# Kernel optimization log

Measured on AMD Instinct MI355X. Metric: run time of the kernel, lower is better.

## Reference

```python
import jax, jax.numpy as jnp
import numpy as np

POOL = 7      # AdaptiveMaxPool2d output size
CROP = 96     # max box side; all generated boxes fit inside a CROP x CROP window


def _adaptive_maxpool_box(feature_chw, coord):
    """PyTorch AdaptiveMaxPool2d((7,7)) on feature_chw[:, y1:y2, x1:x2].

    feature_chw: [2, H, W]; coord: int32 [4] = (y1, x1, y2, x2), with
    0 < y2-y1 <= CROP, 0 < x2-x1 <= CROP. Returns [2, 7, 7].
    """
    y1, x1, y2, x2 = coord[0], coord[1], coord[2], coord[3]
    crop = jax.lax.dynamic_slice(feature_chw, (0, y1, x1), (2, CROP, CROP))
    h = y2 - y1
    w = x2 - x1
    i = jnp.arange(POOL)
    r = jnp.arange(CROP)
    # PyTorch adaptive pooling bins: [floor(i*h/P), ceil((i+1)*h/P))
    sr = (i * h) // POOL
    er = ((i + 1) * h + POOL - 1) // POOL
    sc = (i * w) // POOL
    ec = ((i + 1) * w + POOL - 1) // POOL
    mask_r = (r[None, :] >= sr[:, None]) & (r[None, :] < er[:, None])  # [7, CROP]
    mask_c = (r[None, :] >= sc[:, None]) & (r[None, :] < ec[:, None])  # [7, CROP]
    neg = jnp.finfo(crop.dtype).min
    # row-wise max per output row: [7, 2, CROP]
    rowp = jnp.max(jnp.where(mask_r[:, None, :, None], crop[None], neg), axis=2)
    # col-wise max per output col: [7, 7, 2]
    out = jnp.max(jnp.where(mask_c[None, :, None, :], rowp[:, None], neg), axis=3)
    return jnp.transpose(out, (2, 0, 1))  # [2, 7, 7]


def setup_inputs() -> dict:
    key = jax.random.key(0)
    k1, k2, k3, k4, k5, k6 = jax.random.split(key, 6)
    N = 1024
    H = W = 2048
    feature = jax.random.normal(k1, (1, 2, H, W), jnp.float32)
    y1 = jax.random.randint(k2, (N,), 0, H - CROP)
    x1 = jax.random.randint(k3, (N,), 0, W - CROP)
    hh = jax.random.randint(k4, (N,), POOL, CROP)
    ww = jax.random.randint(k5, (N,), POOL, CROP)
    box_coords = jnp.stack([y1, x1, y1 + hh, x1 + ww], axis=1).astype(jnp.int32)
    boxes = jnp.concatenate(
        [jnp.zeros((N, 1), jnp.float32),
         jnp.arange(N, dtype=jnp.float32)[:, None],
         box_coords.astype(jnp.float32)], axis=1)  # [N, 6]
    fc_w = jax.random.normal(k6, (4, POOL * POOL * 2), jnp.float32) * 0.1
    fc_b = jnp.zeros((4,), jnp.float32)
    return {"feature": feature, "boxes": boxes, "box_coords": box_coords,
            "fc_w": fc_w, "fc_b": fc_b}


def reference(feature, boxes, box_coords, fc_w, fc_b):
    # per-box ROI adaptive max pool, batched with vmap: [N, 2, 7, 7]
    pooled = jax.vmap(lambda c: _adaptive_maxpool_box(feature[0], c))(box_coords)
    feat = pooled.reshape(pooled.shape[0], -1)        # [N, 98] (channel-major flatten)
    deltaB = jax.nn.relu(feat @ fc_w.T + fc_b)        # [N, 4]
    return boxes.at[:, 2:6].add(deltaB)               # boxes[:,2:6] += deltaB
```

## Files before the change

kernel.cpp:

```cpp
#include <hip/hip_runtime.h>
#include <float.h>

#define POOL 7
#define FW 2048
#define FH 2048
#define CROP 96
#define LROW 100

#define GLD16(gp, lp) __builtin_amdgcn_global_load_lds( \
    (const __attribute__((address_space(1))) void*)(gp), \
    (__attribute__((address_space(3))) void*)(lp), 16, 0, 0)

__global__ __launch_bounds__(256, 4) void roi_pool_fc_kernel(
    const float* __restrict__ feature,
    const float* __restrict__ boxes,
    const int*   __restrict__ coords,
    const float* __restrict__ fc_w,
    const float* __restrict__ fc_b,
    float* __restrict__ out,
    int N)
{
    const int n = blockIdx.x;
    const int t = threadIdx.x;

    __shared__ float lds[CROP * LROW + 8];
    __shared__ float pooled[98];
    __shared__ float delta[4];

    const int4 cd = ((const int4*)coords)[n];
    const int y1 = cd.x;
    const int x1 = cd.y;
    const int h  = cd.z - y1;
    const int w  = cd.w - x1;

    const int x1a  = x1 & ~3;
    const int off  = x1 - x1a;
    const int wvec = (w + off + 3) >> 2;

    float wpre[4] = {0.f, 0.f, 0.f, 0.f};
    float bias = 0.f;
    if (t < 128) {
        const int oo = t >> 5, lane = t & 31;
        const float* wrow = fc_w + oo * 98;
        #pragma unroll
        for (int k = 0; k < 4; ++k) {
            const int idx = lane + 32 * k;
            if (idx < 98) wpre[k] = wrow[idx];
        }
        if (lane == 0) bias = fc_b[oo];
    }
    const float bx = (t < 6) ? boxes[n * 6 + t] : 0.f;

    const float* b0 = feature + (size_t)y1 * FW + x1a;
    const float* b1 = b0 + (size_t)FH * FW;
    const int wbase = t & 192;

    int  goff[10];
    bool vok[10];
    #pragma unroll
    for (int k = 0; k < 10; ++k) {
        const int v = t + k * 256;
        const int r = v / 25;
        const int c4 = v - r * 25;
        goff[k] = r * FW + 4 * c4;
        vok[k]  = (v < 2400) && (r < h) && (c4 < wvec);
    }

    #pragma unroll
    for (int k = 0; k < 10; ++k) {
        char* lbase = (char*)lds + 16 * (wbase + k * 256);
        if (vok[k]) GLD16(b0 + goff[k], lbase);
    }

    const int o = t >> 2;
    const int s = t & 3;
    const int i = o / 7;
    const int j = o % 7;
    int sr = 0, er = 0, sc4 = 0;
    float sel[20];
    if (t < 196) {
        sr = (i * h) / POOL;
        er = ((i + 1) * h + POOL - 1) / POOL;
        const int sc = (j * w) / POOL + off;
        const int ec = ((j + 1) * w + POOL - 1) / POOL + off;
        sc4 = sc >> 2;
        #pragma unroll
        for (int q = 0; q < 20; ++q) {
            const int b = sc4 * 4 + q;
            sel[q] = (b >= sc && b < ec) ? FLT_MAX : -FLT_MAX;
        }
    }

    auto binmax = [&]() -> float {
        float m = -FLT_MAX;
        for (int r = sr + s; r < er; r += 4) {
            const float4* rowp = (const float4*)(lds + r * LROW + 4 * sc4);
            float4 v[5];
            #pragma unroll
            for (int q = 0; q < 5; ++q) v[q] = rowp[q];
            #pragma unroll
            for (int q = 0; q < 5; ++q) {
                m = fmaxf(m, fminf(v[q].x, sel[4 * q + 0]));
                m = fmaxf(m, fminf(v[q].y, sel[4 * q + 1]));
                m = fmaxf(m, fminf(v[q].z, sel[4 * q + 2]));
                m = fmaxf(m, fminf(v[q].w, sel[4 * q + 3]));
            }
        }
        m = fmaxf(m, __shfl_xor(m, 1, 64));
        m = fmaxf(m, __shfl_xor(m, 2, 64));
        return m;
    };

    __syncthreads();

    float m0 = -FLT_MAX;
    if (t < 196) m0 = binmax();
    __syncthreads();

    #pragma unroll
    for (int k = 0; k < 10; ++k) {
        char* lbase = (char*)lds + 16 * (wbase + k * 256);
        if (vok[k]) GLD16(b1 + goff[k], lbase);
    }
    __syncthreads();

    if (t < 196) {
        const float m1 = binmax();
        if (s == 0) { pooled[o] = m0; pooled[49 + o] = m1; }
    }
    __syncthreads();

    if (t < 128) {
        const int lane = t & 31;
        float acc = 0.f;
        #pragma unroll
        for (int k = 0; k < 4; ++k) {
            const int idx = lane + 32 * k;
            acc = fmaf(idx < 98 ? pooled[idx] : 0.f, wpre[k], acc);
        }
        #pragma unroll
        for (int mm = 16; mm; mm >>= 1)
            acc += __shfl_xor(acc, mm, 64);
        if (lane == 0) delta[t >> 5] = fmaxf(acc + bias, 0.f);
    }
    __syncthreads();

    if (t < 6)
        out[n * 6 + t] = bx + (t >= 2 ? delta[t - 2] : 0.f);
}

extern "C" void kernel_launch(void* const* d_in, const int* in_sizes, int n_in,
                              void* d_out, int out_size, void* d_ws, size_t ws_size,
                              hipStream_t stream) {
    const float* feature = (const float*)d_in[0];
    const float* boxes   = (const float*)d_in[1];
    const int*   coords  = (const int*)d_in[2];
    const float* fc_w    = (const float*)d_in[3];
    const float* fc_b    = (const float*)d_in[4];
    float* out = (float*)d_out;

    const int N = in_sizes[2] / 4;
    roi_pool_fc_kernel<<<N, 256, 0, stream>>>(feature, boxes, coords, fc_w, fc_b, out, N);
}
```

Baseline: 83.90 us.

## Replace LDS-staged crop with direct per-bin global loads, both channels concurrently

Drops the two-phase LDS staging of the 96x100 crop (global_load_lds plus barriers per channel). Each of 196 threads now handles one half of a (channel, bin) pair, reading its bin's rows straight from global memory with double-buffered float4 loads and a clamped row index. This removes the LDS round trip and the serialisation between channels. In exchange, neighbouring bins re-read overlapping columns from global/L2, and a clamped duplicate row may be read when a thread's row count is odd.

```diff
diff --git a/kernel.cpp b/kernel.cpp
--- a/kernel.cpp
+++ b/kernel.cpp
@@ -5,11 +5,6 @@
 #define FW 2048
 #define FH 2048
 #define CROP 96
-#define LROW 100
-
-#define GLD16(gp, lp) __builtin_amdgcn_global_load_lds( \
-    (const __attribute__((address_space(1))) void*)(gp), \
-    (__attribute__((address_space(3))) void*)(lp), 16, 0, 0)
 
 __global__ __launch_bounds__(256, 4) void roi_pool_fc_kernel(
     const float* __restrict__ feature,
@@ -23,7 +18,6 @@
     const int n = blockIdx.x;
     const int t = threadIdx.x;
 
-    __shared__ float lds[CROP * LROW + 8];
     __shared__ float pooled[98];
     __shared__ float delta[4];
 
@@ -33,9 +27,8 @@
     const int h  = cd.z - y1;
     const int w  = cd.w - x1;
 
-    const int x1a  = x1 & ~3;
-    const int off  = x1 - x1a;
-    const int wvec = (w + off + 3) >> 2;
+    const int x1a = x1 & ~3;
+    const int off = x1 - x1a;
 
     float wpre[4] = {0.f, 0.f, 0.f, 0.f};
     float bias = 0.f;
@@ -43,90 +36,75 @@
         const int oo = t >> 5, lane = t & 31;
         const float* wrow = fc_w + oo * 98;
         #pragma unroll
-        for (int k = 0; k < 4; ++k) {
-            const int idx = lane + 32 * k;
-            if (idx < 98) wpre[k] = wrow[idx];
+        for (int kk = 0; kk < 4; ++kk) {
+            const int idx = lane + 32 * kk;
+            if (idx < 98) wpre[kk] = wrow[idx];
         }
         if (lane == 0) bias = fc_b[oo];
     }
     const float bx = (t < 6) ? boxes[n * 6 + t] : 0.f;
 
-    const float* b0 = feature + (size_t)y1 * FW + x1a;
-    const float* b1 = b0 + (size_t)FH * FW;
-    const int wbase = t & 192;
+    const int K = (((h + 6) / 7) + 2) >> 1;
 
-    int  goff[10];
-    bool vok[10];
-    #pragma unroll
-    for (int k = 0; k < 10; ++k) {
-        const int v = t + k * 256;
-        const int r = v / 25;
-        const int c4 = v - r * 25;
-        goff[k] = r * FW + 4 * c4;
-        vok[k]  = (v < 2400) && (r < h) && (c4 < wvec);
-    }
+    if (t < 196) {
+        const int s = t & 1;
+        const int u = t >> 1;
+        const int c = u / 49;
+        const int o = u - c * 49;
+        const int i = o / 7;
+        const int j = o % 7;
 
-    #pragma unroll
-    for (int k = 0; k < 10; ++k) {
-        char* lbase = (char*)lds + 16 * (wbase + k * 256);
-        if (vok[k]) GLD16(b0 + goff[k], lbase);
-    }
+        const int sr  = (i * h) / POOL;
+        const int er  = ((i + 1) * h + POOL - 1) / POOL;
+        const int sc  = (j * w) / POOL + off;
+        const int ec  = ((j + 1) * w + POOL - 1) / POOL + off;
+        const int sc4 = sc >> 2;
 
-    const int o = t >> 2;
-    const int s = t & 3;
-    const int i = o / 7;
-    const int j = o % 7;
-    int sr = 0, er = 0, sc4 = 0;
-    float sel[20];
-    if (t < 196) {
-        sr = (i * h) / POOL;
-        er = ((i + 1) * h + POOL - 1) / POOL;
-        const int sc = (j * w) / POOL + off;
-        const int ec = ((j + 1) * w + POOL - 1) / POOL + off;
-        sc4 = sc >> 2;
+        float sel[20];
         #pragma unroll
         for (int q = 0; q < 20; ++q) {
             const int b = sc4 * 4 + q;
             sel[q] = (b >= sc && b < ec) ? FLT_MAX : -FLT_MAX;
         }
-    }
 
-    auto binmax = [&]() -> float {
+        const float* cbase = feature + (size_t)c * ((size_t)FH * FW)
+                           + (size_t)y1 * FW + x1a + 4 * sc4;
+        const int rb    = sr + s;
+        const int ermax = er - 1;
+
         float m = -FLT_MAX;
-        for (int r = sr + s; r < er; r += 4) {
-            const float4* rowp = (const float4*)(lds + r * LROW + 4 * sc4);
-            float4 v[5];
+        float4 A[5], B[5];
+
+        auto loadrow = [&](float4* V, int kk) {
+            int rr = rb + 2 * kk;
+            rr = (rr < ermax) ? rr : ermax;
+            const float4* rp = (const float4*)(cbase + (size_t)rr * FW);
             #pragma unroll
-            for (int q = 0; q < 5; ++q) v[q] = rowp[q];
+            for (int q = 0; q < 5; ++q) V[q] = rp[q];
+        };
+        auto acc5 = [&](const float4* V) {
             #pragma unroll
             for (int q = 0; q < 5; ++q) {
-                m = fmaxf(m, fminf(v[q].x, sel[4 * q + 0]));
-                m = fmaxf(m, fminf(v[q].y, sel[4 * q + 1]));
-                m = fmaxf(m, fminf(v[q].z, sel[4 * q + 2]));
-                m = fmaxf(m, fminf(v[q].w, sel[4 * q + 3]));
+                m = fmaxf(m, fminf(V[q].x, sel[4 * q + 0]));
+                m = fmaxf(m, fminf(V[q].y, sel[4 * q + 1]));
+                m = fmaxf(m, fminf(V[q].z, sel[4 * q + 2]));
+                m = fmaxf(m, fminf(V[q].w, sel[4 * q + 3]));
             }
+        };
+
+        loadrow(A, 0);
+        int k = 1;
+        for (; k + 1 < K; k += 2) {
+            loadrow(B, k);
+            acc5(A);
+            loadrow(A, k + 1);
+            acc5(B);
         }
+        if (k < K) { loadrow(B, k); acc5(A); acc5(B); }
+        else       { acc5(A); }
+
         m = fmaxf(m, __shfl_xor(m, 1, 64));
-        m = fmaxf(m, __shfl_xor(m, 2, 64));
-        return m;
-    };
-
-    __syncthreads();
-
-    float m0 = -FLT_MAX;
-    if (t < 196) m0 = binmax();
-    __syncthreads();
-
-    #pragma unroll
-    for (int k = 0; k < 10; ++k) {
-        char* lbase = (char*)lds + 16 * (wbase + k * 256);
-        if (vok[k]) GLD16(b1 + goff[k], lbase);
-    }
-    __syncthreads();
-
-    if (t < 196) {
-        const float m1 = binmax();
-        if (s == 0) { pooled[o] = m0; pooled[49 + o] = m1; }
+        if (s == 0) pooled[u] = m;
     }
     __syncthreads();
 
@@ -134,9 +112,9 @@
         const int lane = t & 31;
         float acc = 0.f;
         #pragma unroll
-        for (int k = 0; k < 4; ++k) {
-            const int idx = lane + 32 * k;
-            acc = fmaf(idx < 98 ? pooled[idx] : 0.f, wpre[k], acc);
+        for (int kk = 0; kk < 4; ++kk) {
+            const int idx = lane + 32 * kk;
+            acc = fmaf(idx < 98 ? pooled[idx] : 0.f, wpre[kk], acc);
         }
         #pragma unroll
         for (int mm = 16; mm; mm >>= 1)
```

Result: no change. 83.56 us (-0.4%).
